# Kernel tuning notes

Measured on AMD Instinct MI355X. Metric: run time of the kernel, lower is better.

The kernel has to match this reference:

```python
import jax, jax.numpy as jnp
import numpy as np

B, L, D_MODEL = 2, 1024, 512
D_INNER, D_STATE, DT_RANK, D_CONV = 1024, 16, 32, 4
N_LAYER, VOCAB, EMBED_DIM, NUM_EMOTIONS = 2, 30000, 256, 7


def setup_inputs() -> dict:
    key = jax.random.key(0)
    ks = jax.random.split(key, 12)
    def n(k, shape, scale=0.02):
        return jax.random.normal(k, shape, jnp.float32) * scale
    A_init = jnp.broadcast_to(jnp.arange(1, D_STATE + 1, dtype=jnp.float32), (N_LAYER, D_INNER, D_STATE))
    return {
        "input_ids": jax.random.randint(ks[0], (B, L), 0, VOCAB),
        "embedding": n(ks[1], (VOCAB, D_MODEL)),
        "norm_w": jnp.ones((N_LAYER, D_MODEL)),
        "in_proj_w": n(ks[2], (N_LAYER, D_MODEL, 2 * D_INNER)),
        "conv_w": n(ks[3], (N_LAYER, D_INNER, 1, D_CONV), 0.1),
        "conv_b": jnp.zeros((N_LAYER, D_INNER)),
        "x_proj_w": n(ks[4], (N_LAYER, D_INNER, DT_RANK + 2 * D_STATE)),
        "dt_proj_w": n(ks[5], (N_LAYER, DT_RANK, D_INNER), 0.1),
        "dt_proj_b": jnp.zeros((N_LAYER, D_INNER)),
        "A_log": jnp.log(A_init),
        "D": jnp.ones((N_LAYER, D_INNER)),
        "out_proj_w": n(ks[6], (N_LAYER, D_INNER, D_MODEL)),
        "norm_f_w": jnp.ones((D_MODEL,)),
        "proj_w": n(ks[7], (D_MODEL, EMBED_DIM)),
        "proj_b": jnp.zeros((EMBED_DIM,)),
        "cls_w": n(ks[8], (EMBED_DIM, NUM_EMOTIONS)),
        "cls_b": jnp.zeros((NUM_EMOTIONS,)),
    }


def rmsnorm(x, w, eps=1e-5):
    return x * jax.lax.rsqrt(jnp.mean(x * x, axis=-1, keepdims=True) + eps) * w


def selective_scan(u, delta, A, B_, C, D_):
    # u, delta: [b,l,d]; A: [d,n]; B_, C: [b,l,n]; D_: [d]
    dA = jnp.exp(jnp.einsum('bld,dn->bldn', delta, A))          # [b,l,d,n]
    dBu = jnp.einsum('bld,bln,bld->bldn', delta, B_, u)          # [b,l,d,n]
    def step(h, inp):
        dA_t, dBu_t, C_t = inp                                   # [b,d,n],[b,d,n],[b,n]
        h = dA_t * h + dBu_t
        y = jnp.einsum('bdn,bn->bd', h, C_t)
        return h, y
    h0 = jnp.zeros((u.shape[0], u.shape[2], A.shape[1]), u.dtype)
    _, ys = jax.lax.scan(step, h0, (dA.transpose(1, 0, 2, 3), dBu.transpose(1, 0, 2, 3), C.transpose(1, 0, 2)))
    return ys.transpose(1, 0, 2) + u * D_                        # [b,l,d]


def mamba_block(x, in_w, cw, cb, xp_w, dt_w, dt_b, A_log, D_, out_w):
    # x: [b,l,d_model]
    xr = x @ in_w                                                # [b,l,2*d_inner]
    xi, res = jnp.split(xr, 2, axis=-1)
    # causal depthwise conv1d over time
    xc = jax.lax.conv_general_dilated(
        xi.transpose(0, 2, 1), cw, window_strides=(1,),
        padding=[(D_CONV - 1, 0)], feature_group_count=D_INNER,
        dimension_numbers=('NCH', 'OIH', 'NCH'))
    xi = jax.nn.silu(xc.transpose(0, 2, 1) + cb)                 # [b,l,d_inner]
    x_dbl = xi @ xp_w
    delta, B_, C = jnp.split(x_dbl, [DT_RANK, DT_RANK + D_STATE], axis=-1)
    delta = jax.nn.softplus(delta @ dt_w + dt_b)                 # [b,l,d_inner]
    A = -jnp.exp(A_log)
    y = selective_scan(xi, delta, A, B_, C, D_)
    y = y * jax.nn.silu(res)
    return y @ out_w                                             # [b,l,d_model]


def reference(input_ids, embedding, norm_w, in_proj_w, conv_w, conv_b, x_proj_w,
              dt_proj_w, dt_proj_b, A_log, D, out_proj_w, norm_f_w,
              proj_w, proj_b, cls_w, cls_b):
    x = embedding[input_ids]                                     # [b,l,d_model]
    for i in range(N_LAYER):
        x = x + mamba_block(rmsnorm(x, norm_w[i]), in_proj_w[i], conv_w[i],
                            conv_b[i], x_proj_w[i], dt_proj_w[i], dt_proj_b[i],
                            A_log[i], D[i], out_proj_w[i])
    x = rmsnorm(x, norm_f_w)
    pooled = x.mean(axis=1)                                      # [b,d_model]
    emotion_emb = pooled @ proj_w + proj_b                       # [b,embed_dim]
    logits = emotion_emb @ cls_w + cls_b                         # [b,num_emotions]
    return logits, emotion_emb
```

## Files before the change

kernel.cpp:

```cpp
#include <hip/hip_runtime.h>
#include <cstddef>

#define D_MODEL   512
#define D_INNER   1024
#define D_STATE   16
#define DT_RANK   32
#define SEQ_L     1024
#define BATCH     2
#define NLAYER    2
#define M_ROWS    (BATCH * SEQ_L)
#define NC        64
#define LC        (SEQ_L / NC)

typedef __bf16 bf16x8 __attribute__((ext_vector_type(8)));
typedef float  f32x4  __attribute__((ext_vector_type(4)));

__device__ __forceinline__ float softplus_f(float x) {
    return fmaxf(x, 0.f) + log1pf(expf(-fabsf(x)));
}
__device__ __forceinline__ float silu_f(float x) {
    return x / (1.f + __expf(-x));
}
__device__ __forceinline__ unsigned short f2bf(float f) {
    unsigned u = __float_as_uint(f);
    return (unsigned short)((u + 0x7fffu + ((u >> 16) & 1u)) >> 16);
}
__device__ __forceinline__ float bf2f(unsigned short v) {
    return __uint_as_float(((unsigned)v) << 16);
}
__device__ __forceinline__ unsigned pack_bf2(float lo, float hi) {
    return (unsigned)f2bf(lo) | ((unsigned)f2bf(hi) << 16);
}

__global__ __launch_bounds__(256) void init_kernel(const int* __restrict__ ids,
                                                   const float* __restrict__ emb,
                                                   const float* __restrict__ in_w,
                                                   const float* __restrict__ out_w,
                                                   float* __restrict__ x,
                                                   unsigned short* __restrict__ in_wt_all,
                                                   unsigned short* __restrict__ out_wt_all) {
    int z = blockIdx.z;
    if (z == 4) {
        int blk = blockIdx.y * 64 + blockIdx.x;
        if (blk >= 1024) return;
        int g = blk * 256 + threadIdx.x;
        int c = (g & 127) << 2;
        int m = g >> 7;
        int row = ids[m];
        *(float4*)&x[(size_t)m * D_MODEL + c] =
            *(const float4*)&emb[(size_t)row * D_MODEL + c];
        return;
    }
    const float* W; unsigned short* Wt; int K, N;
    if (z < 2) {
        if (blockIdx.x >= 64 || blockIdx.y >= 16) return;
        W = in_w + (size_t)z * 512 * 2048; Wt = in_wt_all + (size_t)z * 2048 * 512;
        K = 512; N = 2048;
    } else {
        int zz = z - 2;
        if (blockIdx.x >= 16 || blockIdx.y >= 32) return;
        W = out_w + (size_t)zz * 1024 * 512; Wt = out_wt_all + (size_t)zz * 512 * 1024;
        K = 1024; N = 512;
    }
    __shared__ float tile[32][33];
    int n0 = blockIdx.x * 32, k0 = blockIdx.y * 32;
    int tx = threadIdx.x & 31, ty = threadIdx.x >> 5;
    #pragma unroll
    for (int i = 0; i < 4; ++i)
        tile[ty + i*8][tx] = W[(size_t)(k0 + ty + i*8) * N + n0 + tx];
    __syncthreads();
    #pragma unroll
    for (int i = 0; i < 4; ++i)
        Wt[(size_t)(n0 + ty + i*8) * K + k0 + tx] = f2bf(tile[tx][ty + i*8]);
}

__global__ __launch_bounds__(64) void rmsnorm_bf_kernel(const float* __restrict__ x,
                                                        const float* __restrict__ w,
                                                        unsigned short* __restrict__ out) {
    int row = blockIdx.x;
    int tid = threadIdx.x;
    const float* xp = x + (size_t)row * D_MODEL;
    float4 v0 = *(const float4*)&xp[tid * 4];
    float4 v1 = *(const float4*)&xp[256 + tid * 4];
    float ss = v0.x*v0.x + v0.y*v0.y + v0.z*v0.z + v0.w*v0.w
             + v1.x*v1.x + v1.y*v1.y + v1.z*v1.z + v1.w*v1.w;
    #pragma unroll
    for (int off = 32; off > 0; off >>= 1) ss += __shfl_xor(ss, off);
    float scale = rsqrtf(ss * (1.f / D_MODEL) + 1e-5f);
    float4 w0 = *(const float4*)&w[tid * 4];
    float4 w1 = *(const float4*)&w[256 + tid * 4];
    unsigned short* op = out + (size_t)row * D_MODEL;
    uint2 p0, p1;
    p0.x = pack_bf2(v0.x * scale * w0.x, v0.y * scale * w0.y);
    p0.y = pack_bf2(v0.z * scale * w0.z, v0.w * scale * w0.w);
    p1.x = pack_bf2(v1.x * scale * w1.x, v1.y * scale * w1.y);
    p1.y = pack_bf2(v1.z * scale * w1.z, v1.w * scale * w1.w);
    *(uint2*)&op[tid * 4] = p0;
    *(uint2*)&op[256 + tid * 4] = p1;
}

__global__ __launch_bounds__(256) void gemm_mfma128(const unsigned short* __restrict__ A,
                                                    const unsigned short* __restrict__ Bt,
                                                    unsigned short* __restrict__ Cb,
                                                    int K, int ldc) {
    __shared__ unsigned short As[128 * 64];
    __shared__ unsigned short Bs[128 * 64];
    int m0 = blockIdx.y * 128;
    int n0 = blockIdx.x * 128;
    int t = threadIdx.x;
    int lane = t & 63, wave = t >> 6;
    int wr = wave >> 1, wc = wave & 1;
    int srow = t >> 3;
    int sc8  = t & 7;
    f32x4 acc[4][4] = {};

    for (int k0 = 0; k0 < K; k0 += 64) {
        __syncthreads();
        #pragma unroll
        for (int i = 0; i < 4; ++i) {
            int row = i * 32 + srow;
            int csrc = sc8 ^ (row & 7);
            __builtin_amdgcn_global_load_lds(
                (const __attribute__((address_space(1))) void*)
                    &A[(size_t)(m0 + row) * K + k0 + csrc * 8],
                (__attribute__((address_space(3))) void*)
                    &As[row * 64 + sc8 * 8], 16, 0, 0);
            __builtin_amdgcn_global_load_lds(
                (const __attribute__((address_space(1))) void*)
                    &Bt[(size_t)(n0 + row) * K + k0 + csrc * 8],
                (__attribute__((address_space(3))) void*)
                    &Bs[row * 64 + sc8 * 8], 16, 0, 0);
        }
        __syncthreads();
        #pragma unroll
        for (int ks = 0; ks < 2; ++ks) {
            bf16x8 av[4], bv[4];
            #pragma unroll
            for (int f = 0; f < 4; ++f) {
                int ar = wr * 64 + f * 16 + (lane & 15);
                int ac = (ks * 4 + (lane >> 4)) ^ (ar & 7);
                av[f] = *reinterpret_cast<const bf16x8*>(&As[ar * 64 + ac * 8]);
                int br = wc * 64 + f * 16 + (lane & 15);
                int bc = (ks * 4 + (lane >> 4)) ^ (br & 7);
                bv[f] = *reinterpret_cast<const bf16x8*>(&Bs[br * 64 + bc * 8]);
            }
            #pragma unroll
            for (int fm = 0; fm < 4; ++fm)
                #pragma unroll
                for (int fn = 0; fn < 4; ++fn)
                    acc[fm][fn] = __builtin_amdgcn_mfma_f32_16x16x32_bf16(
                        av[fm], bv[fn], acc[fm][fn], 0, 0, 0);
        }
    }
    #pragma unroll
    for (int fm = 0; fm < 4; ++fm)
        #pragma unroll
        for (int fn = 0; fn < 4; ++fn) {
            int row = m0 + wr * 64 + fm * 16 + (lane >> 4) * 4;
            int col = n0 + wc * 64 + fn * 16 + (lane & 15);
            #pragma unroll
            for (int r = 0; r < 4; ++r)
                Cb[(size_t)(row + r) * ldc + col] = f2bf(acc[fm][fn][r]);
        }
}

__global__ __launch_bounds__(256) void gemm_mfma64_acc(const unsigned short* __restrict__ A,
                                                       const unsigned short* __restrict__ Bt,
                                                       float* __restrict__ C,
                                                       int K, int ldc) {
    __shared__ unsigned short As[64 * 64];
    __shared__ unsigned short Bs[64 * 64];
    int m0 = blockIdx.y * 64;
    int n0 = blockIdx.x * 64;
    int t = threadIdx.x;
    int lane = t & 63, wave = t >> 6;
    int wr = wave >> 1, wc = wave & 1;
    int srow = t >> 3;
    int sc8  = t & 7;
    f32x4 acc[2][2] = {};

    for (int k0 = 0; k0 < K; k0 += 64) {
        __syncthreads();
        #pragma unroll
        for (int i = 0; i < 2; ++i) {
            int row = i * 32 + srow;
            int csrc = sc8 ^ (row & 7);
            __builtin_amdgcn_global_load_lds(
                (const __attribute__((address_space(1))) void*)
                    &A[(size_t)(m0 + row) * K + k0 + csrc * 8],
                (__attribute__((address_space(3))) void*)
                    &As[row * 64 + sc8 * 8], 16, 0, 0);
            __builtin_amdgcn_global_load_lds(
                (const __attribute__((address_space(1))) void*)
                    &Bt[(size_t)(n0 + row) * K + k0 + csrc * 8],
                (__attribute__((address_space(3))) void*)
                    &Bs[row * 64 + sc8 * 8], 16, 0, 0);
        }
        __syncthreads();
        #pragma unroll
        for (int ks = 0; ks < 2; ++ks) {
            bf16x8 av[2], bv[2];
            #pragma unroll
            for (int f = 0; f < 2; ++f) {
                int ar = wr * 32 + f * 16 + (lane & 15);
                int ac = (ks * 4 + (lane >> 4)) ^ (ar & 7);
                av[f] = *reinterpret_cast<const bf16x8*>(&As[ar * 64 + ac * 8]);
                int br = wc * 32 + f * 16 + (lane & 15);
                int bc = (ks * 4 + (lane >> 4)) ^ (br & 7);
                bv[f] = *reinterpret_cast<const bf16x8*>(&Bs[br * 64 + bc * 8]);
            }
            #pragma unroll
            for (int fm = 0; fm < 2; ++fm)
                #pragma unroll
                for (int fn = 0; fn < 2; ++fn)
                    acc[fm][fn] = __builtin_amdgcn_mfma_f32_16x16x32_bf16(
                        av[fm], bv[fn], acc[fm][fn], 0, 0, 0);
        }
    }
    #pragma unroll
    for (int fm = 0; fm < 2; ++fm)
        #pragma unroll
        for (int fn = 0; fn < 2; ++fn) {
            int row = m0 + wr * 32 + fm * 16 + (lane >> 4) * 4;
            int col = n0 + wc * 32 + fn * 16 + (lane & 15);
            #pragma unroll
            for (int r = 0; r < 4; ++r)
                C[(size_t)(row + r) * ldc + col] += acc[fm][fn][r];
        }
}

__global__ void conv_bf_kernel(const unsigned short* __restrict__ xi,
                               const float* __restrict__ cw,
                               const float* __restrict__ cb,
                               unsigned short* __restrict__ u) {
    int g = blockIdx.x * blockDim.x + threadIdx.x;
    int d = g & (D_INNER - 1);
    int m = g >> 10;
    int l = m & (SEQ_L - 1);
    float4 w = *(const float4*)&cw[d * 4];
    const unsigned short* col = &xi[(size_t)m * 2048 + d];
    float x3 = bf2f(col[0]);
    float x2 = (l >= 1) ? bf2f(col[-2048]) : 0.f;
    float x1 = (l >= 2) ? bf2f(col[-4096]) : 0.f;
    float x0 = (l >= 3) ? bf2f(col[-6144]) : 0.f;
    u[g] = f2bf(silu_f(cb[d] + w.x*x0 + w.y*x1 + w.z*x2 + w.w*x3));
}

__global__ __launch_bounds__(256) void xproj_kernel(const unsigned short* __restrict__ u,
                                                    const float* __restrict__ Bw,
                                                    float* __restrict__ Cc) {
    __shared__ float Bsh[64][68];
    __shared__ float Ash[4][64];
    int row0 = blockIdx.x * 4;
    int t = threadIdx.x;
    int tr = t >> 6, c = t & 63;
    int kk = t >> 2, cb4 = (t & 3) << 4;
    float acc = 0.f;
    for (int k0 = 0; k0 < 1024; k0 += 64) {
        __syncthreads();
        #pragma unroll
        for (int j = 0; j < 4; ++j) {
            float4 v = *(const float4*)&Bw[(size_t)(k0 + kk) * 64 + cb4 + j * 4];
            *(float4*)&Bsh[kk][cb4 + j * 4] = v;
        }
        Ash[tr][c] = bf2f(u[(size_t)(row0 + tr) * 1024 + k0 + c]);
        __syncthreads();
        #pragma unroll
        for (int k = 0; k < 64; ++k)
            acc = fmaf(Ash[tr][k], Bsh[k][c], acc);
    }
    Cc[(size_t)(row0 + tr) * 64 + c] = acc;
}

#define BM 64
#define BN 64
#define BKK 16
__global__ __launch_bounds__(256) void gemm_dt(const float* __restrict__ A,
                                               const float* __restrict__ Bm,
                                               const float* __restrict__ bias,
                                               float* __restrict__ C,
                                               int lda, int ldb, int ldc) {
    __shared__ float As[BM][BKK + 4];
    __shared__ float Bs[BKK][BN];
    int tid = threadIdx.x;
    int n0 = blockIdx.x * BN;
    int m0 = blockIdx.y * BM;
    int tx4 = (tid & 15) << 2;
    int ty4 = (tid >> 4) << 2;
    int arow = tid >> 2, akk = (tid & 3) << 2;
    int brow = tid >> 4, bcol = (tid & 15) << 2;
    float acc[4][4] = {};
    for (int k0 = 0; k0 < 32; k0 += BKK) {
        float4 av = *(const float4*)&A[(size_t)(m0 + arow) * lda + k0 + akk];
        float4 bv = *(const float4*)&Bm[(size_t)(k0 + brow) * ldb + n0 + bcol];
        *(float4*)&As[arow][akk] = av;
        *(float4*)&Bs[brow][bcol] = bv;
        __syncthreads();
        #pragma unroll
        for (int k = 0; k < BKK; ++k) {
            float a0 = As[ty4 + 0][k];
            float a1 = As[ty4 + 1][k];
            float a2 = As[ty4 + 2][k];
            float a3 = As[ty4 + 3][k];
            float4 b = *(float4*)&Bs[k][tx4];
            acc[0][0] = fmaf(a0, b.x, acc[0][0]); acc[0][1] = fmaf(a0, b.y, acc[0][1]);
            acc[0][2] = fmaf(a0, b.z, acc[0][2]); acc[0][3] = fmaf(a0, b.w, acc[0][3]);
            acc[1][0] = fmaf(a1, b.x, acc[1][0]); acc[1][1] = fmaf(a1, b.y, acc[1][1]);
            acc[1][2] = fmaf(a1, b.z, acc[1][2]); acc[1][3] = fmaf(a1, b.w, acc[1][3]);
            acc[2][0] = fmaf(a2, b.x, acc[2][0]); acc[2][1] = fmaf(a2, b.y, acc[2][1]);
            acc[2][2] = fmaf(a2, b.z, acc[2][2]); acc[2][3] = fmaf(a2, b.w, acc[2][3]);
            acc[3][0] = fmaf(a3, b.x, acc[3][0]); acc[3][1] = fmaf(a3, b.y, acc[3][1]);
            acc[3][2] = fmaf(a3, b.z, acc[3][2]); acc[3][3] = fmaf(a3, b.w, acc[3][3]);
        }
        __syncthreads();
    }
    #pragma unroll
    for (int i = 0; i < 4; ++i) {
        int m = m0 + ty4 + i;
        float4 bb = *(const float4*)&bias[n0 + tx4];
        float4 v = make_float4(softplus_f(acc[i][0] + bb.x), softplus_f(acc[i][1] + bb.y),
                               softplus_f(acc[i][2] + bb.z), softplus_f(acc[i][3] + bb.w));
        *(float4*)&C[(size_t)m * ldc + n0 + tx4] = v;
    }
}

__global__ __launch_bounds__(256) void scan_p1i(const unsigned short* __restrict__ u,
                                                const float* __restrict__ delta,
                                                const float* __restrict__ xdbl,
                                                const float* __restrict__ A_log,
                                                float* __restrict__ aprod,
                                                float* __restrict__ hloc) {
    int tid = threadIdx.x;
    int d = blockIdx.x * 256 + tid;
    int b = blockIdx.y, c = blockIdx.z;
    int l0 = c * LC;
    __shared__ float sBC[LC][32];
    for (int i = tid; i < LC * 32; i += 256) {
        int l = i >> 5, j = i & 31;
        sBC[l][j] = xdbl[(size_t)(b * SEQ_L + l0 + l) * 64 + 32 + j];
    }
    __syncthreads();
    float A_[D_STATE], h[D_STATE], ap[D_STATE];
    #pragma unroll
    for (int n = 0; n < D_STATE; ++n) {
        A_[n] = -__expf(A_log[(size_t)d * D_STATE + n]);
        h[n] = 0.f; ap[n] = 1.f;
    }
    const unsigned short* ucol = u + (size_t)(b * SEQ_L + l0) * D_INNER + d;
    const float* dcol = delta + (size_t)(b * SEQ_L + l0) * D_INNER + d;
    for (int l = 0; l < LC; ++l) {
        float dtv = dcol[l * D_INNER];
        float uu = bf2f(ucol[l * D_INNER]);
        float du = dtv * uu;
        #pragma unroll
        for (int n = 0; n < D_STATE; ++n) {
            float e = __expf(dtv * A_[n]);
            h[n] = fmaf(e, h[n], du * sBC[l][n]);
            ap[n] *= e;
        }
    }
    #pragma unroll
    for (int n = 0; n < D_STATE; ++n) {
        size_t o = (((size_t)b * NC + c) * D_STATE + n) * D_INNER + d;
        aprod[o] = ap[n];
        hloc[o] = h[n];
    }
}

__global__ __launch_bounds__(256) void scan_p2(const float* __restrict__ aprod,
                                               float* __restrict__ hloc) {
    int d = blockIdx.x * 256 + threadIdx.x;
    int n = blockIdx.y;
    int b = blockIdx.z;
    float h = 0.f;
    #pragma unroll 4
    for (int c = 0; c < NC; ++c) {
        size_t o = (((size_t)b * NC + c) * D_STATE + n) * D_INNER + d;
        float ap = aprod[o];
        float lc = hloc[o];
        hloc[o] = h;
        h = fmaf(ap, h, lc);
    }
}

__global__ __launch_bounds__(256) void scan_p3i(const unsigned short* __restrict__ u,
                                                const float* __restrict__ delta,
                                                const float* __restrict__ xdbl,
                                                const float* __restrict__ A_log,
                                                const float* __restrict__ Dp,
                                                const float* __restrict__ hinit,
                                                const unsigned short* __restrict__ xi,
                                                unsigned short* __restrict__ y) {
    int tid = threadIdx.x;
    int d = blockIdx.x * 256 + tid;
    int b = blockIdx.y, c = blockIdx.z;
    int l0 = c * LC;
    __shared__ float sBC[LC][32];
    for (int i = tid; i < LC * 32; i += 256) {
        int l = i >> 5, j = i & 31;
        sBC[l][j] = xdbl[(size_t)(b * SEQ_L + l0 + l) * 64 + 32 + j];
    }
    __syncthreads();
    float A_[D_STATE], h[D_STATE];
    #pragma unroll
    for (int n = 0; n < D_STATE; ++n) {
        A_[n] = -__expf(A_log[(size_t)d * D_STATE + n]);
        size_t o = (((size_t)b * NC + c) * D_STATE + n) * D_INNER + d;
        h[n] = hinit[o];
    }
    float Dd = Dp[d];
    const unsigned short* ucol = u  + (size_t)(b * SEQ_L + l0) * D_INNER + d;
    const float* dcol = delta + (size_t)(b * SEQ_L + l0) * D_INNER + d;
    const unsigned short* rcol = xi + (size_t)(b * SEQ_L + l0) * 2048 + 1024 + d;
    for (int l = 0; l < LC; ++l) {
        float dtv = dcol[l * D_INNER];
        float uu = bf2f(ucol[l * D_INNER]);
        float du = dtv * uu;
        float yv = 0.f;
        #pragma unroll
        for (int n = 0; n < D_STATE; ++n) {
            float e = __expf(dtv * A_[n]);
            h[n] = fmaf(e, h[n], du * sBC[l][n]);
            yv = fmaf(h[n], sBC[l][16 + n], yv);
        }
        yv = fmaf(uu, Dd, yv);
        float res = bf2f(rcol[l * 2048]);
        y[(size_t)(b * SEQ_L + l0 + l) * D_INNER + d] = f2bf(yv * silu_f(res));
    }
}

__global__ __launch_bounds__(256) void rms_pool1(const float* __restrict__ x,
                                                 float* __restrict__ partial) {
    int blk = blockIdx.x;
    int b = blk >> 5, c = blk & 31;
    int wave = threadIdx.x >> 6, lane = threadIdx.x & 63;
    int row0 = b * SEQ_L + c * 32 + wave * 8;
    float4 a0 = make_float4(0.f, 0.f, 0.f, 0.f);
    float4 a1 = make_float4(0.f, 0.f, 0.f, 0.f);
    for (int r = 0; r < 8; ++r) {
        const float* xp = x + (size_t)(row0 + r) * D_MODEL;
        float4 v0 = *(const float4*)&xp[lane * 4];
        float4 v1 = *(const float4*)&xp[256 + lane * 4];
        float ss = v0.x*v0.x + v0.y*v0.y + v0.z*v0.z + v0.w*v0.w
                 + v1.x*v1.x + v1.y*v1.y + v1.z*v1.z + v1.w*v1.w;
        #pragma unroll
        for (int off = 32; off > 0; off >>= 1) ss += __shfl_xor(ss, off);
        float s = rsqrtf(ss * (1.f / D_MODEL) + 1e-5f);
        a0.x = fmaf(v0.x, s, a0.x); a0.y = fmaf(v0.y, s, a0.y);
        a0.z = fmaf(v0.z, s, a0.z); a0.w = fmaf(v0.w, s, a0.w);
        a1.x = fmaf(v1.x, s, a1.x); a1.y = fmaf(v1.y, s, a1.y);
        a1.z = fmaf(v1.z, s, a1.z); a1.w = fmaf(v1.w, s, a1.w);
    }
    __shared__ float red[4][512];
    *(float4*)&red[wave][lane * 4] = a0;
    *(float4*)&red[wave][256 + lane * 4] = a1;
    __syncthreads();
    int d = threadIdx.x * 2;
    float s0 = red[0][d] + red[1][d] + red[2][d] + red[3][d];
    float s1 = red[0][d+1] + red[1][d+1] + red[2][d+1] + red[3][d+1];
    partial[(size_t)blk * 512 + d]     = s0;
    partial[(size_t)blk * 512 + d + 1] = s1;
}

__global__ __launch_bounds__(512) void tail2_kernel(const float* __restrict__ ppart,
                                                    const float* __restrict__ w,
                                                    const float* __restrict__ pw,
                                                    const float* __restrict__ pb,
                                                    const float* __restrict__ cw,
                                                    const float* __restrict__ cb,
                                                    float* __restrict__ out) {
    __shared__ float sp[2][512];
    __shared__ float se[2][256];
    int t = threadIdx.x;
    {
        int b = t >> 8, dp = (t & 255) * 2;
        float s0 = 0.f, s1 = 0.f;
        #pragma unroll 8
        for (int c = 0; c < 32; ++c) {
            const float* pp = &ppart[((size_t)b * 32 + c) * 512 + dp];
            s0 += pp[0]; s1 += pp[1];
        }
        sp[b][dp]     = s0 * (1.f / SEQ_L) * w[dp];
        sp[b][dp + 1] = s1 * (1.f / SEQ_L) * w[dp + 1];
    }
    __syncthreads();
    {
        int b = t >> 8, e = t & 255;
        float acc = pb[e];
        #pragma unroll 8
        for (int k = 0; k < 512; ++k)
            acc = fmaf(sp[b][k], pw[(size_t)k * 256 + e], acc);
        out[14 + b * 256 + e] = acc;
        se[b][e] = acc;
    }
    __syncthreads();
    {
        int wave = t >> 6, lane = t & 63;
        for (int idx = wave; idx < 14; idx += 8) {
            int bb = idx / 7, cc = idx % 7;
            float a = 0.f;
            #pragma unroll
            for (int i = 0; i < 4; ++i) {
                int k = lane + i * 64;
                a = fmaf(se[bb][k], cw[k * 7 + cc], a);
            }
            #pragma unroll
            for (int off = 32; off > 0; off >>= 1) a += __shfl_xor(a, off);
            if (lane == 0) out[bb * 7 + cc] = a + cb[cc];
        }
    }
}

extern "C" void kernel_launch(void* const* d_in, const int* in_sizes, int n_in,
                              void* d_out, int out_size, void* d_ws, size_t ws_size,
                              hipStream_t stream) {
    const int*   ids    = (const int*)d_in[0];
    const float* emb    = (const float*)d_in[1];
    const float* norm_w = (const float*)d_in[2];
    const float* in_w   = (const float*)d_in[3];
    const float* conv_w = (const float*)d_in[4];
    const float* conv_b = (const float*)d_in[5];
    const float* xp_w   = (const float*)d_in[6];
    const float* dt_w   = (const float*)d_in[7];
    const float* dt_b   = (const float*)d_in[8];
    const float* A_log  = (const float*)d_in[9];
    const float* Dp     = (const float*)d_in[10];
    const float* out_w  = (const float*)d_in[11];
    const float* normf  = (const float*)d_in[12];
    const float* proj_w = (const float*)d_in[13];
    const float* proj_b = (const float*)d_in[14];
    const float* cls_w  = (const float*)d_in[15];
    const float* cls_b  = (const float*)d_in[16];
    float* out = (float*)d_out;

    float* p = (float*)d_ws;
    float* x      = p; p += 1 << 20;
    float* xnr    = p; p += 1 << 20;
    float* xrr    = p; p += 2 << 20;
    float* urr    = p; p += 1 << 20;
    float* deltab = p; p += 2 << 20;
    float* xdbl   = p; p += 1 << 17;
    float* wreg   = p; p += 1572864;
    float* aprod  = p; p += 2 << 20;
    float* hloc   = p; p += 2 << 20;
    float* ybr    = p; p += 1 << 20;

    unsigned short* xn_bf  = (unsigned short*)xnr;
    float*          ppart  = xnr;
    unsigned short* xr_bf  = (unsigned short*)xrr;
    unsigned short* u_bf   = (unsigned short*)urr;
    unsigned short* in_wt_all  = (unsigned short*)wreg;
    unsigned short* out_wt_all = (unsigned short*)(wreg + (1 << 20));
    unsigned short* yb_bf  = (unsigned short*)ybr;

    init_kernel<<<dim3(64, 32, 5), 256, 0, stream>>>(
        ids, emb, in_w, out_w, x, in_wt_all, out_wt_all);

    for (int i = 0; i < NLAYER; ++i) {
        unsigned short* in_wt  = in_wt_all  + (size_t)i * 2048 * 512;
        unsigned short* out_wt = out_wt_all + (size_t)i * 512 * 1024;
        const float* cwi  = conv_w + (size_t)i * D_INNER * 4;
        const float* cbi  = conv_b + (size_t)i * D_INNER;
        const float* dtwi = dt_w + (size_t)i * DT_RANK * D_INNER;
        const float* dtbi = dt_b + (size_t)i * D_INNER;
        const float* Ali  = A_log + (size_t)i * D_INNER * D_STATE;
        const float* Dpi  = Dp + (size_t)i * D_INNER;

        rmsnorm_bf_kernel<<<M_ROWS, 64, 0, stream>>>(x, norm_w + i * D_MODEL, xn_bf);
        gemm_mfma128<<<dim3(2048 / 128, M_ROWS / 128), 256, 0, stream>>>(
            xn_bf, in_wt, xr_bf, 512, 2048);
        conv_bf_kernel<<<(M_ROWS * D_INNER) / 256, 256, 0, stream>>>(
            xr_bf, cwi, cbi, u_bf);
        xproj_kernel<<<M_ROWS / 4, 256, 0, stream>>>(
            u_bf, xp_w + (size_t)i * D_INNER * 64, xdbl);
        gemm_dt<<<dim3(1024 / BN, M_ROWS / BM), 256, 0, stream>>>(
            xdbl, dtwi, dtbi, deltab, 64, 1024, 1024);
        scan_p1i<<<dim3(4, BATCH, NC), 256, 0, stream>>>(
            u_bf, deltab, xdbl, Ali, aprod, hloc);
        scan_p2<<<dim3(4, D_STATE, BATCH), 256, 0, stream>>>(aprod, hloc);
        scan_p3i<<<dim3(4, BATCH, NC), 256, 0, stream>>>(
            u_bf, deltab, xdbl, Ali, Dpi, hloc, xr_bf, yb_bf);
        gemm_mfma64_acc<<<dim3(512 / 64, M_ROWS / 64), 256, 0, stream>>>(
            yb_bf, out_wt, x, 1024, 512);
    }

    rms_pool1<<<BATCH * 32, 256, 0, stream>>>(x, ppart);
    tail2_kernel<<<1, 512, 0, stream>>>(ppart, normf, proj_w, proj_b, cls_w, cls_b, out);
}
```

Baseline: 254.9 us.

## Fuse causal conv, x-projection and dt-projection into one kernel

Replaces three kernels (depthwise conv+SiLU, x_proj GEMV, dt_proj GEMM with softplus) with a single kernel per 4-row block. The conv output is kept in shared memory in fp32 and fed straight to the x-projection, whose 64 outputs then drive the dt projection. This removes two launches and the re-read of u and xdbl from global memory. In exchange, each block re-reads the full dt_proj weights from global or cache and uses about 20KB of shared memory, which may lower occupancy. The dt GEMM also loses its tiling.

```diff
diff --git a/kernel.cpp b/kernel.cpp
--- a/kernel.cpp
+++ b/kernel.cpp
@@ -229,98 +229,66 @@
         }
 }
 
-__global__ void conv_bf_kernel(const unsigned short* __restrict__ xi,
-                               const float* __restrict__ cw,
-                               const float* __restrict__ cb,
-                               unsigned short* __restrict__ u) {
-    int g = blockIdx.x * blockDim.x + threadIdx.x;
-    int d = g & (D_INNER - 1);
-    int m = g >> 10;
-    int l = m & (SEQ_L - 1);
-    float4 w = *(const float4*)&cw[d * 4];
-    const unsigned short* col = &xi[(size_t)m * 2048 + d];
-    float x3 = bf2f(col[0]);
-    float x2 = (l >= 1) ? bf2f(col[-2048]) : 0.f;
-    float x1 = (l >= 2) ? bf2f(col[-4096]) : 0.f;
-    float x0 = (l >= 3) ? bf2f(col[-6144]) : 0.f;
-    u[g] = f2bf(silu_f(cb[d] + w.x*x0 + w.y*x1 + w.z*x2 + w.w*x3));
-}
-
-__global__ __launch_bounds__(256) void xproj_kernel(const unsigned short* __restrict__ u,
-                                                    const float* __restrict__ Bw,
-                                                    float* __restrict__ Cc) {
+__global__ __launch_bounds__(256) void cxd_fused(const unsigned short* __restrict__ xi,
+                                                 const float* __restrict__ cw,
+                                                 const float* __restrict__ cb,
+                                                 const float* __restrict__ xpw,
+                                                 const float* __restrict__ dtw,
+                                                 const float* __restrict__ dtb,
+                                                 unsigned short* __restrict__ u,
+                                                 float* __restrict__ xdbl,
+                                                 float* __restrict__ delta) {
+    __shared__ float sU[4][1024];
     __shared__ float Bsh[64][68];
-    __shared__ float Ash[4][64];
+    __shared__ float sX[4][64];
     int row0 = blockIdx.x * 4;
     int t = threadIdx.x;
+
+    #pragma unroll
+    for (int j = 0; j < 16; ++j) {
+        int idx = j * 256 + t;
+        int r = idx >> 10, d = idx & 1023;
+        int m = row0 + r;
+        int l = m & (SEQ_L - 1);
+        float4 w = *(const float4*)&cw[d * 4];
+        const unsigned short* col = &xi[(size_t)m * 2048 + d];
+        float x3 = bf2f(col[0]);
+        float x2 = (l >= 1) ? bf2f(col[-2048]) : 0.f;
+        float x1 = (l >= 2) ? bf2f(col[-4096]) : 0.f;
+        float x0 = (l >= 3) ? bf2f(col[-6144]) : 0.f;
+        float uu = silu_f(cb[d] + w.x*x0 + w.y*x1 + w.z*x2 + w.w*x3);
+        sU[r][d] = uu;
+        u[(size_t)m * D_INNER + d] = f2bf(uu);
+    }
+    __syncthreads();
+
     int tr = t >> 6, c = t & 63;
     int kk = t >> 2, cb4 = (t & 3) << 4;
     float acc = 0.f;
     for (int k0 = 0; k0 < 1024; k0 += 64) {
         __syncthreads();
         #pragma unroll
-        for (int j = 0; j < 4; ++j) {
-            float4 v = *(const float4*)&Bw[(size_t)(k0 + kk) * 64 + cb4 + j * 4];
-            *(float4*)&Bsh[kk][cb4 + j * 4] = v;
-        }
-        Ash[tr][c] = bf2f(u[(size_t)(row0 + tr) * 1024 + k0 + c]);
+        for (int jj = 0; jj < 4; ++jj)
+            *(float4*)&Bsh[kk][cb4 + jj * 4] =
+                *(const float4*)&xpw[(size_t)(k0 + kk) * 64 + cb4 + jj * 4];
         __syncthreads();
         #pragma unroll
         for (int k = 0; k < 64; ++k)
-            acc = fmaf(Ash[tr][k], Bsh[k][c], acc);
-    }
-    Cc[(size_t)(row0 + tr) * 64 + c] = acc;
-}
-
-#define BM 64
-#define BN 64
-#define BKK 16
-__global__ __launch_bounds__(256) void gemm_dt(const float* __restrict__ A,
-                                               const float* __restrict__ Bm,
-                                               const float* __restrict__ bias,
-                                               float* __restrict__ C,
-                                               int lda, int ldb, int ldc) {
-    __shared__ float As[BM][BKK + 4];
-    __shared__ float Bs[BKK][BN];
-    int tid = threadIdx.x;
-    int n0 = blockIdx.x * BN;
-    int m0 = blockIdx.y * BM;
-    int tx4 = (tid & 15) << 2;
-    int ty4 = (tid >> 4) << 2;
-    int arow = tid >> 2, akk = (tid & 3) << 2;
-    int brow = tid >> 4, bcol = (tid & 15) << 2;
-    float acc[4][4] = {};
-    for (int k0 = 0; k0 < 32; k0 += BKK) {
-        float4 av = *(const float4*)&A[(size_t)(m0 + arow) * lda + k0 + akk];
-        float4 bv = *(const float4*)&Bm[(size_t)(k0 + brow) * ldb + n0 + bcol];
-        *(float4*)&As[arow][akk] = av;
-        *(float4*)&Bs[brow][bcol] = bv;
-        __syncthreads();
-        #pragma unroll
-        for (int k = 0; k < BKK; ++k) {
-            float a0 = As[ty4 + 0][k];
-            float a1 = As[ty4 + 1][k];
-            float a2 = As[ty4 + 2][k];
-            float a3 = As[ty4 + 3][k];
-            float4 b = *(float4*)&Bs[k][tx4];
-            acc[0][0] = fmaf(a0, b.x, acc[0][0]); acc[0][1] = fmaf(a0, b.y, acc[0][1]);
-            acc[0][2] = fmaf(a0, b.z, acc[0][2]); acc[0][3] = fmaf(a0, b.w, acc[0][3]);
-            acc[1][0] = fmaf(a1, b.x, acc[1][0]); acc[1][1] = fmaf(a1, b.y, acc[1][1]);
-            acc[1][2] = fmaf(a1, b.z, acc[1][2]); acc[1][3] = fmaf(a1, b.w, acc[1][3]);
-            acc[2][0] = fmaf(a2, b.x, acc[2][0]); acc[2][1] = fmaf(a2, b.y, acc[2][1]);
-            acc[2][2] = fmaf(a2, b.z, acc[2][2]); acc[2][3] = fmaf(a2, b.w, acc[2][3]);
-            acc[3][0] = fmaf(a3, b.x, acc[3][0]); acc[3][1] = fmaf(a3, b.y, acc[3][1]);
-            acc[3][2] = fmaf(a3, b.z, acc[3][2]); acc[3][3] = fmaf(a3, b.w, acc[3][3]);
-        }
-        __syncthreads();
-    }
-    #pragma unroll
-    for (int i = 0; i < 4; ++i) {
-        int m = m0 + ty4 + i;
-        float4 bb = *(const float4*)&bias[n0 + tx4];
-        float4 v = make_float4(softplus_f(acc[i][0] + bb.x), softplus_f(acc[i][1] + bb.y),
-                               softplus_f(acc[i][2] + bb.z), softplus_f(acc[i][3] + bb.w));
-        *(float4*)&C[(size_t)m * ldc + n0 + tx4] = v;
+            acc = fmaf(sU[tr][k0 + k], Bsh[k][c], acc);
+    }
+    xdbl[(size_t)(row0 + tr) * 64 + c] = acc;
+    sX[tr][c] = acc;
+    __syncthreads();
+
+    #pragma unroll
+    for (int j = 0; j < 16; ++j) {
+        int idx = j * 256 + t;
+        int r = idx >> 10, d = idx & 1023;
+        float dtv = dtb[d];
+        #pragma unroll
+        for (int k = 0; k < 32; ++k)
+            dtv = fmaf(sX[r][k], dtw[k * 1024 + d], dtv);
+        delta[(size_t)(row0 + r) * D_INNER + d] = softplus_f(dtv);
     }
 }
 
@@ -569,12 +537,9 @@
         rmsnorm_bf_kernel<<<M_ROWS, 64, 0, stream>>>(x, norm_w + i * D_MODEL, xn_bf);
         gemm_mfma128<<<dim3(2048 / 128, M_ROWS / 128), 256, 0, stream>>>(
             xn_bf, in_wt, xr_bf, 512, 2048);
-        conv_bf_kernel<<<(M_ROWS * D_INNER) / 256, 256, 0, stream>>>(
-            xr_bf, cwi, cbi, u_bf);
-        xproj_kernel<<<M_ROWS / 4, 256, 0, stream>>>(
-            u_bf, xp_w + (size_t)i * D_INNER * 64, xdbl);
-        gemm_dt<<<dim3(1024 / BN, M_ROWS / BM), 256, 0, stream>>>(
-            xdbl, dtwi, dtbi, deltab, 64, 1024, 1024);
+        cxd_fused<<<M_ROWS / 4, 256, 0, stream>>>(
+            xr_bf, cwi, cbi, xp_w + (size_t)i * D_INNER * 64, dtwi, dtbi,
+            u_bf, xdbl, deltab);
         scan_p1i<<<dim3(4, BATCH, NC), 256, 0, stream>>>(
             u_bf, deltab, xdbl, Ali, aprod, hloc);
         scan_p2<<<dim3(4, D_STATE, BATCH), 256, 0, stream>>>(aprod, hloc);
```

New measurement: 385.7 us. +51.3%, slower.
